# Kernel optimization log

Measured on AMD Instinct MI355X. Metric: run time of the kernel, lower is better.

Reference implementation:

```python
import jax, jax.numpy as jnp
import numpy as np

B, N, C, H = 8, 1024, 768, 12
HD = C // H  # 64
SCALE = HD ** -0.5
T = 4
N_HALF = T // 2  # loop body with attention runs N_HALF times, V accumulates T times


def setup_inputs() -> dict:
    key = jax.random.key(0)
    ks = jax.random.split(key, 8)
    s = 0.02
    return {
        "x": jax.random.normal(ks[0], (B, N, C), jnp.float32),
        "Wqkv": jax.random.normal(ks[1], (3 * C, C), jnp.float32) * s,
        "Wfc1": jax.random.normal(ks[2], (HD, HD), jnp.float32) * s,
        "bfc1": jax.random.normal(ks[3], (HD,), jnp.float32) * s,
        "Wfc2": jax.random.normal(ks[4], (HD, HD), jnp.float32) * s,
        "bfc2": jax.random.normal(ks[5], (HD,), jnp.float32) * s,
        "Wproj": jax.random.normal(ks[6], (C, C), jnp.float32) * s,
        "bproj": jax.random.normal(ks[7], (C,), jnp.float32) * s,
    }


def reference(x, Wqkv, Wfc1, bfc1, Wfc2, bfc2, Wproj, bproj):
    b, n, c = x.shape
    # qkv projection (no bias), split into per-head q,k,v: [B,H,N,hd]
    qkv = (x @ Wqkv.T).reshape(b, n, 3, H, HD).transpose(2, 0, 3, 1, 4)
    q, k, v = qkv[0], qkv[1], qkv[2]
    # Loop body is stateless per timestep: first N_HALF steps each add the same
    # att_spk; all T steps add the same relu(v). Compute once, scale by counts.
    Q_spk = jax.nn.relu(q) @ Wfc1.T + bfc1  # [B,H,N,hd]
    K_spk = jax.nn.relu(k) @ Wfc2.T + bfc2  # [B,H,N,hd]
    att_spk = jax.nn.relu(jnp.einsum("bhqd,bhkd->bhqk", Q_spk, K_spk) * SCALE)
    att_rec = att_spk * float(N_HALF)   # accumulated over t < T/2
    V_rec = jax.nn.relu(v) * float(T)   # accumulated over all T steps
    att = jax.nn.softmax(att_rec, axis=-1)
    out = jnp.einsum("bhqk,bhkd->bhqd", att, V_rec)  # [B,H,N,hd]
    out = out.transpose(0, 2, 1, 3).reshape(b, n, c)
    return out @ Wproj.T + bproj
```

## Files before the change

kernel.cpp:

```cpp
#include <hip/hip_runtime.h>
#include <hip/hip_bf16.h>
#include <stdint.h>
#include <math.h>

#define BB   8
#define NN_  1024
#define CC   768
#define HH   12
#define HDD  64

typedef __attribute__((ext_vector_type(8))) short bf16x8;
typedef __attribute__((ext_vector_type(4))) float f32x4;
typedef __attribute__((ext_vector_type(16))) float f32x16;
typedef __attribute__((ext_vector_type(4))) float f32x4v;
typedef __attribute__((ext_vector_type(4))) unsigned short u16x4;

union FragU { unsigned int u[4]; bf16x8 b; };

__device__ __forceinline__ unsigned short f2bf(float f) {
    union { float f; unsigned int u; } v; v.f = f;
    unsigned int r = v.u + 0x7fffu + ((v.u >> 16) & 1u);
    return (unsigned short)(r >> 16);
}

#define CVTPK(d_, a_, b_) asm("v_cvt_pk_bf16_f32 %0, %1, %2" : "=v"(d_) : "v"(a_), "v"(b_))
#define SWAP32(a_, b_) asm("v_permlane32_swap_b32 %0, %1" : "+v"(a_), "+v"(b_))

#define GLDS(g_, l_) __builtin_amdgcn_global_load_lds( \
    (const __attribute__((address_space(1))) void*)(g_), \
    (__attribute__((address_space(3))) void*)(l_), 16, 0, 0)

#define MKFRAGS(P_, F0_, F1_) do {                                             \
    unsigned int c0,c1,c2,c3,c4,c5,c6,c7;                                      \
    CVTPK(c0, P_[0],  P_[1]);  CVTPK(c1, P_[2],  P_[3]);                       \
    CVTPK(c2, P_[4],  P_[5]);  CVTPK(c3, P_[6],  P_[7]);                       \
    CVTPK(c4, P_[8],  P_[9]);  CVTPK(c5, P_[10], P_[11]);                      \
    CVTPK(c6, P_[12], P_[13]); CVTPK(c7, P_[14], P_[15]);                      \
    SWAP32(c0, c2); SWAP32(c1, c3); SWAP32(c4, c6); SWAP32(c5, c7);            \
    FragU fu0_, fu1_;                                                          \
    fu0_.u[0]=c0; fu0_.u[1]=c1; fu0_.u[2]=c2; fu0_.u[3]=c3;                    \
    fu1_.u[0]=c4; fu1_.u[1]=c5; fu1_.u[2]=c6; fu1_.u[3]=c7;                    \
    F0_ = fu0_.b; F1_ = fu1_.b;                                                \
} while (0)

#define CVT_N0 1572864
#define CVT_N1 2015232
#define CVT_N2 2162688
#define CVT_N3 2163712
#define CVT_N4 2164736
__global__ void cvt_all(const float* __restrict__ x, const float* __restrict__ wqkv,
                        const float* __restrict__ wproj, const float* __restrict__ wf1,
                        const float* __restrict__ wf2,
                        unsigned short* __restrict__ xb, unsigned short* __restrict__ wqkvb,
                        unsigned short* __restrict__ wprojb, unsigned short* __restrict__ wf1b,
                        unsigned short* __restrict__ wf2b) {
    int i = blockIdx.x * blockDim.x + threadIdx.x;
    int stride = gridDim.x * blockDim.x;
    for (; i < CVT_N4; i += stride) {
        const f32x4v* src; u16x4* dst; int off;
        if (i < CVT_N0)      { src = (const f32x4v*)x;     dst = (u16x4*)xb;     off = i; }
        else if (i < CVT_N1) { src = (const f32x4v*)wqkv;  dst = (u16x4*)wqkvb;  off = i - CVT_N0; }
        else if (i < CVT_N2) { src = (const f32x4v*)wproj; dst = (u16x4*)wprojb; off = i - CVT_N1; }
        else if (i < CVT_N3) { src = (const f32x4v*)wf1;   dst = (u16x4*)wf1b;   off = i - CVT_N2; }
        else                 { src = (const f32x4v*)wf2;   dst = (u16x4*)wf2b;   off = i - CVT_N3; }
        f32x4v v = src[off];
        u16x4 o;
        o.x = f2bf(v.x); o.y = f2bf(v.y); o.z = f2bf(v.z); o.w = f2bf(v.w);
        dst[off] = o;
    }
}

__global__ __launch_bounds__(256)
void qkv_spk_gemm(const unsigned short* __restrict__ X,
                  const unsigned short* __restrict__ Wqkv,
                  const unsigned short* __restrict__ Wf1,
                  const unsigned short* __restrict__ Wf2,
                  const float* __restrict__ bf1,
                  const float* __restrict__ bf2,
                  unsigned short* __restrict__ Rq,
                  unsigned short* __restrict__ Rk,
                  unsigned short* __restrict__ VT) {
    __shared__ short sX[128 * 32];
    __shared__ short sW[128 * 32];
    const int K = 768;
    const int t    = threadIdx.x;
    const int wid  = t >> 6;
    const int lane = t & 63;
    const int l31  = lane & 31;
    const int hi5  = lane >> 5;
    const int th = (wid & 1) * 64;
    const int fh = (wid >> 1) * 64;
    const int brow = blockIdx.x * 128;
    const int bcol = blockIdx.y * 128;

    const int srow = t >> 2;
    const int scol = ((t & 3) ^ (srow & 3)) * 8;

#define QSTG(k0_) do {                                                         \
    _Pragma("unroll")                                                          \
    for (int i = 0; i < 2; i++) {                                              \
        int row_ = srow + i * 64;                                              \
        GLDS(X    + (size_t)(brow + row_) * K + (k0_) + scol,                  \
             &sX[(i * 256 + wid * 64) * 8]);                                   \
        GLDS(Wqkv + (size_t)(bcol + row_) * K + (k0_) + scol,                  \
             &sW[(i * 256 + wid * 64) * 8]);                                   \
    }                                                                          \
} while (0)

    f32x16 acc[2][2];
#pragma unroll
    for (int fb = 0; fb < 2; fb++)
#pragma unroll
        for (int tb = 0; tb < 2; tb++)
#pragma unroll
            for (int r = 0; r < 16; r++) acc[fb][tb][r] = 0.f;

    for (int k0 = 0; k0 < K; k0 += 32) {
        QSTG(k0);
        __syncthreads();
        const char* cw = (const char*)sW;
        const char* cx = (const char*)sX;
        bf16x8 wf[2][2], xf[2][2];
#pragma unroll
        for (int fb = 0; fb < 2; fb++) {
            int row = fh + fb * 32 + l31;
            const char* rb = cw + row * 64;
#pragma unroll
            for (int kk = 0; kk < 2; kk++)
                wf[fb][kk] = *(const bf16x8*)(rb + (((kk * 2 + hi5) ^ (row & 3)) << 4));
        }
#pragma unroll
        for (int tb = 0; tb < 2; tb++) {
            int row = th + tb * 32 + l31;
            const char* rb = cx + row * 64;
#pragma unroll
            for (int kk = 0; kk < 2; kk++)
                xf[tb][kk] = *(const bf16x8*)(rb + (((kk * 2 + hi5) ^ (row & 3)) << 4));
        }
#pragma unroll
        for (int kk = 0; kk < 2; kk++)
#pragma unroll
            for (int fb = 0; fb < 2; fb++)
#pragma unroll
                for (int tb = 0; tb < 2; tb++)
                    acc[fb][tb] = __builtin_amdgcn_mfma_f32_32x32x16_bf16(
                        wf[fb][kk], xf[tb][kk], acc[fb][tb], 0, 0, 0);
        __syncthreads();
    }
#undef QSTG

    const int fbase = bcol + fh;
    const int p  = fbase / 768;
    const int hh = (fbase - p * 768) >> 6;
    const int tok0 = brow + th;
    const int b  = tok0 >> 10;
    const int n0 = tok0 & 1023;
    const int crow0 = 4 * hi5;

    if (p == 2) {
        const size_t vtb = ((size_t)(b * HH + hh)) * HDD * NN_;
#pragma unroll
        for (int fb = 0; fb < 2; fb++)
#pragma unroll
            for (int tb = 0; tb < 2; tb++)
#pragma unroll
                for (int r = 0; r < 16; r++) {
                    int d = fb * 32 + (r & 3) + 8 * (r >> 2) + crow0;
                    int n = n0 + tb * 32 + l31;
                    VT[vtb + (size_t)d * NN_ + n] = f2bf(4.f * fmaxf(acc[fb][tb][r], 0.f));
                }
    } else {
        const unsigned short* Wf = p ? Wf2 : Wf1;
        const float* bfp = p ? bf2 : bf1;
        unsigned short* R = p ? Rk : Rq;
        bf16x8 wfr[2][4];
#pragma unroll
        for (int dh = 0; dh < 2; dh++)
#pragma unroll
            for (int ks = 0; ks < 4; ks++)
                wfr[dh][ks] = *(const bf16x8*)&Wf[(size_t)(dh * 32 + l31) * HDD + ks * 16 + hi5 * 8];
        float bv0 = bfp[l31], bv1 = bfp[32 + l31];
        const size_t qkb = ((size_t)(b * HH + hh)) * NN_ * HDD;
#pragma unroll
        for (int tb = 0; tb < 2; tb++) {
            float pv0[16], pv1[16];
#pragma unroll
            for (int r = 0; r < 16; r++) {
                pv0[r] = fmaxf(acc[0][tb][r], 0.f);
                pv1[r] = fmaxf(acc[1][tb][r], 0.f);
            }
            bf16x8 pa0, pa1, pa2, pa3;
            MKFRAGS(pv0, pa0, pa1);
            MKFRAGS(pv1, pa2, pa3);
            f32x16 D0, D1;
#pragma unroll
            for (int r = 0; r < 16; r++) { D0[r] = 0.f; D1[r] = 0.f; }
            D0 = __builtin_amdgcn_mfma_f32_32x32x16_bf16(pa0, wfr[0][0], D0, 0, 0, 0);
            D0 = __builtin_amdgcn_mfma_f32_32x32x16_bf16(pa1, wfr[0][1], D0, 0, 0, 0);
            D0 = __builtin_amdgcn_mfma_f32_32x32x16_bf16(pa2, wfr[0][2], D0, 0, 0, 0);
            D0 = __builtin_amdgcn_mfma_f32_32x32x16_bf16(pa3, wfr[0][3], D0, 0, 0, 0);
            D1 = __builtin_amdgcn_mfma_f32_32x32x16_bf16(pa0, wfr[1][0], D1, 0, 0, 0);
            D1 = __builtin_amdgcn_mfma_f32_32x32x16_bf16(pa1, wfr[1][1], D1, 0, 0, 0);
            D1 = __builtin_amdgcn_mfma_f32_32x32x16_bf16(pa2, wfr[1][2], D1, 0, 0, 0);
            D1 = __builtin_amdgcn_mfma_f32_32x32x16_bf16(pa3, wfr[1][3], D1, 0, 0, 0);
#pragma unroll
            for (int r = 0; r < 16; r++) {
                int n = n0 + tb * 32 + (r & 3) + 8 * (r >> 2) + crow0;
                size_t rowb = qkb + (size_t)n * HDD;
                R[rowb + l31]      = f2bf(D0[r] + bv0);
                R[rowb + 32 + l31] = f2bf(D1[r] + bv1);
            }
        }
    }
}

__global__ __launch_bounds__(256, 2)
void attn_kernel(const unsigned short* __restrict__ Q,
                 const unsigned short* __restrict__ Kx,
                 const unsigned short* __restrict__ VT,
                 unsigned short* __restrict__ AO) {
    __shared__ short sK[2][64 * 64];
    __shared__ short sV[2][64 * 64];
    __shared__ float sinv[4][32];

    const int t    = threadIdx.x;
    const int lane = t & 63;
    const int wid  = t >> 6;
    const int l31  = lane & 31;
    const int hi5  = lane >> 5;

    const int bid = (int)blockIdx.x;
    const int lbid = (bid & 7) * 96 + (bid >> 3);
    const int bh = lbid >> 3;
    const int qt = lbid & 7;
    const int b = bh / HH, h = bh - b * HH;

    const unsigned short* Qs = Q  + (size_t)bh * NN_ * HDD;
    const unsigned short* Ks = Kx + (size_t)bh * NN_ * HDD;
    const unsigned short* Vt = VT + (size_t)bh * HDD * NN_;
    const int q0 = qt * 128 + wid * 32;

    bf16x8 qf[4];
#pragma unroll
    for (int ds = 0; ds < 4; ds++)
        qf[ds] = *(const bf16x8*)&Qs[(size_t)(q0 + l31) * HDD + ds * 16 + hi5 * 8];

    f32x16 O0, O1;
#pragma unroll
    for (int r = 0; r < 16; r++) { O0[r] = 0.f; O1[r] = 0.f; }
    float sumacc = 0.f;

    const int srow = t >> 3;
    const int sslot = t & 7;
    const int dstoff = ((t & 192)) * 8;

#define STAGE(buf_, kt_) do {                                                  \
    _Pragma("unroll")                                                          \
    for (int i = 0; i < 2; i++) {                                              \
        int row_ = srow + i * 32;                                              \
        int sl_  = (sslot ^ (row_ & 7)) << 3;                                  \
        const unsigned short* gk_ = Ks + (size_t)((kt_) * 64 + row_) * HDD + sl_; \
        const unsigned short* gv_ = Vt + (size_t)row_ * NN_ + (kt_) * 64 + sl_;   \
        GLDS(gk_, &sK[buf_][i * 2048 + dstoff]);                               \
        GLDS(gv_, &sV[buf_][i * 2048 + dstoff]);                               \
    }                                                                          \
} while (0)

    STAGE(0, 0);
    __syncthreads();

    int buf = 0;
    for (int kt = 0; kt < 16; ++kt) {
        if (kt < 15) STAGE(buf ^ 1, kt + 1);

        const char* kbase = (const char*)&sK[buf][0];
        const char* vbase = (const char*)&sV[buf][0];

        bf16x8 vbf[4][2];
#pragma unroll
        for (int ks = 0; ks < 4; ks++)
#pragma unroll
            for (int dt = 0; dt < 2; dt++) {
                int d = dt * 32 + l31;
                vbf[ks][dt] = *(const bf16x8*)(vbase + d * 128 +
                               ((ks * 32 + hi5 * 16) ^ ((d & 7) << 4)));
            }
        bf16x8 ka[2][4];
#pragma unroll
        for (int kt2 = 0; kt2 < 2; kt2++)
#pragma unroll
            for (int ds = 0; ds < 4; ds++) {
                int kk = kt2 * 32 + l31;
                ka[kt2][ds] = *(const bf16x8*)(kbase + kk * 128 +
                               ((ds * 32 + hi5 * 16) ^ ((kk & 7) << 4)));
            }

        f32x16 S0, S1;
#pragma unroll
        for (int r = 0; r < 16; r++) { S0[r] = 0.f; S1[r] = 0.f; }
#pragma unroll
        for (int ds = 0; ds < 4; ds++) {
            S0 = __builtin_amdgcn_mfma_f32_32x32x16_bf16(ka[0][ds], qf[ds], S0, 0, 0, 0);
            S1 = __builtin_amdgcn_mfma_f32_32x32x16_bf16(ka[1][ds], qf[ds], S1, 0, 0, 0);
        }

        float p0[16], p1[16];
#pragma unroll
        for (int r = 0; r < 16; r++) {
            p0[r] = exp2f(0.36067376f * fmaxf(S0[r], 0.f));
            p1[r] = exp2f(0.36067376f * fmaxf(S1[r], 0.f));
        }
        float s0 = 0.f, s1 = 0.f;
#pragma unroll
        for (int r = 0; r < 16; r++) { s0 += p0[r]; s1 += p1[r]; }
        sumacc += s0 + s1;

        bf16x8 paf0, paf1, paf2, paf3;
        MKFRAGS(p0, paf0, paf1);
        MKFRAGS(p1, paf2, paf3);

        O0 = __builtin_amdgcn_mfma_f32_32x32x16_bf16(paf0, vbf[0][0], O0, 0, 0, 0);
        O1 = __builtin_amdgcn_mfma_f32_32x32x16_bf16(paf0, vbf[0][1], O1, 0, 0, 0);
        O0 = __builtin_amdgcn_mfma_f32_32x32x16_bf16(paf1, vbf[1][0], O0, 0, 0, 0);
        O1 = __builtin_amdgcn_mfma_f32_32x32x16_bf16(paf1, vbf[1][1], O1, 0, 0, 0);
        O0 = __builtin_amdgcn_mfma_f32_32x32x16_bf16(paf2, vbf[2][0], O0, 0, 0, 0);
        O1 = __builtin_amdgcn_mfma_f32_32x32x16_bf16(paf2, vbf[2][1], O1, 0, 0, 0);
        O0 = __builtin_amdgcn_mfma_f32_32x32x16_bf16(paf3, vbf[3][0], O0, 0, 0, 0);
        O1 = __builtin_amdgcn_mfma_f32_32x32x16_bf16(paf3, vbf[3][1], O1, 0, 0, 0);

        __syncthreads();
        buf ^= 1;
    }
#undef STAGE

    float stot = sumacc + __shfl_xor(sumacc, 32, 64);
    float inv = 1.f / stot;
    if (l31 == lane) sinv[wid][l31] = inv;
    __syncthreads();

#pragma unroll
    for (int r = 0; r < 16; r++) {
        int qloc = (r & 3) + 8 * (r >> 2) + 4 * hi5;
        float iv = sinv[wid][qloc];
        size_t row = (size_t)(b * NN_ + q0 + qloc) * CC + h * HDD;
        AO[row + l31]      = f2bf(O0[r] * iv);
        AO[row + 32 + l31] = f2bf(O1[r] * iv);
    }
}

__global__ __launch_bounds__(256)
void proj_gemm(const unsigned short* __restrict__ A,
               const unsigned short* __restrict__ Bt,
               const float* __restrict__ bias,
               float* __restrict__ Out) {
    __shared__ short sA[128 * 32];
    __shared__ short sB[128 * 32];
    const int K = 768;
    const int lane = threadIdx.x & 63;
    const int wid  = threadIdx.x >> 6;
    const int wr = wid >> 1, wc = wid & 1;
    const int brow = blockIdx.x * 128;
    const int bcol = blockIdx.y * 128;
    const int t = threadIdx.x;

    f32x4 acc[4][4];
#pragma unroll
    for (int m = 0; m < 4; m++)
#pragma unroll
        for (int n = 0; n < 4; n++) acc[m][n] = (f32x4){0.f, 0.f, 0.f, 0.f};

    for (int k0 = 0; k0 < K; k0 += 32) {
#pragma unroll
        for (int i = 0; i < 2; i++) {
            int tt  = i * 256 + t;
            int row = tt >> 2;
            int kc  = (tt & 3) * 8;
            const unsigned short* ga = A  + (size_t)(brow + row) * K + k0 + kc;
            const unsigned short* gb = Bt + (size_t)(bcol + row) * K + k0 + kc;
            GLDS(ga, &sA[(i * 256 + wid * 64) * 8]);
            GLDS(gb, &sB[(i * 256 + wid * 64) * 8]);
        }
        __syncthreads();
        bf16x8 af[4], bfg[4];
#pragma unroll
        for (int m = 0; m < 4; m++) {
            int r = wr * 64 + m * 16 + (lane & 15);
            af[m] = *(const bf16x8*)&sA[r * 32 + (lane >> 4) * 8];
        }
#pragma unroll
        for (int n = 0; n < 4; n++) {
            int c = wc * 64 + n * 16 + (lane & 15);
            bfg[n] = *(const bf16x8*)&sB[c * 32 + (lane >> 4) * 8];
        }
#pragma unroll
        for (int m = 0; m < 4; m++)
#pragma unroll
            for (int n = 0; n < 4; n++)
                acc[m][n] = __builtin_amdgcn_mfma_f32_16x16x32_bf16(af[m], bfg[n], acc[m][n], 0, 0, 0);
        __syncthreads();
    }
#pragma unroll
    for (int m = 0; m < 4; m++)
#pragma unroll
        for (int n = 0; n < 4; n++) {
            int col = bcol + wc * 64 + n * 16 + (lane & 15);
            float bv = bias[col];
#pragma unroll
            for (int r = 0; r < 4; r++) {
                int row = brow + wr * 64 + m * 16 + (lane >> 4) * 4 + r;
                Out[(size_t)row * 768 + col] = acc[m][n][r] + bv;
            }
        }
}

extern "C" void kernel_launch(void* const* d_in, const int* in_sizes, int n_in,
                              void* d_out, int out_size, void* d_ws, size_t ws_size,
                              hipStream_t stream) {
    const float* x     = (const float*)d_in[0];
    const float* Wqkv  = (const float*)d_in[1];
    const float* Wfc1  = (const float*)d_in[2];
    const float* bfc1  = (const float*)d_in[3];
    const float* Wfc2  = (const float*)d_in[4];
    const float* bfc2  = (const float*)d_in[5];
    const float* Wproj = (const float*)d_in[6];
    const float* bproj = (const float*)d_in[7];
    float* out = (float*)d_out;

    char* ws = (char*)d_ws;
    const size_t SZ_XN = (size_t)8192 * 768 * 2;
    unsigned short* x_bf    = (unsigned short*)ws; ws += SZ_XN;
    unsigned short* wqkv_bf = (unsigned short*)ws; ws += (size_t)2304 * 768 * 2;
    unsigned short* wproj_bf= (unsigned short*)ws; ws += (size_t)768 * 768 * 2;
    unsigned short* wfc1_bf = (unsigned short*)ws; ws += 64 * 64 * 2;
    unsigned short* wfc2_bf = (unsigned short*)ws; ws += 64 * 64 * 2;
    unsigned short* Rq      = (unsigned short*)ws; ws += SZ_XN;
    unsigned short* Rk      = (unsigned short*)ws; ws += SZ_XN;
    unsigned short* VT      = (unsigned short*)ws; ws += SZ_XN;

    cvt_all<<<2048, 256, 0, stream>>>(x, Wqkv, Wproj, Wfc1, Wfc2,
                                      x_bf, wqkv_bf, wproj_bf, wfc1_bf, wfc2_bf);
    qkv_spk_gemm<<<dim3(64, 18), 256, 0, stream>>>(x_bf, wqkv_bf, wfc1_bf, wfc2_bf,
                                                   bfc1, bfc2, Rq, Rk, VT);
    attn_kernel<<<768, 256, 0, stream>>>(Rq, Rk, VT, x_bf);
    proj_gemm<<<dim3(64, 6), 256, 0, stream>>>(x_bf, wproj_bf, bproj, out);
}
```

Before: 144.9 us.

## Restructure QKV GEMM with 256x128 tiles, triple-buffered LDS pipeline, and XCD-aware block mapping

Rewrites the QKV projection GEMM to use 512-thread blocks with 256x128 output tiles and BK=64. Global-to-LDS loads run through a three-stage ring buffer, issued two tiles ahead and waited on with vmcnt, so there is one barrier per tile instead of two. The block index is remapped across the 8 XCDs for better L2 locality, and MFMA priority is raised with setprio. This trades higher LDS use (about 144KB) and one block per CU for fewer syncs and more overlap of loads with compute.

```diff
diff --git a/kernel.cpp b/kernel.cpp
--- a/kernel.cpp
+++ b/kernel.cpp
@@ -70,7 +70,7 @@
     }
 }
 
-__global__ __launch_bounds__(256)
+__global__ __launch_bounds__(512, 1)
 void qkv_spk_gemm(const unsigned short* __restrict__ X,
                   const unsigned short* __restrict__ Wqkv,
                   const unsigned short* __restrict__ Wf1,
@@ -80,30 +80,39 @@
                   unsigned short* __restrict__ Rq,
                   unsigned short* __restrict__ Rk,
                   unsigned short* __restrict__ VT) {
-    __shared__ short sX[128 * 32];
-    __shared__ short sW[128 * 32];
-    const int K = 768;
+    __shared__ short sA[3][256 * 64];
+    __shared__ short sB[3][128 * 64];
+
     const int t    = threadIdx.x;
     const int wid  = t >> 6;
     const int lane = t & 63;
     const int l31  = lane & 31;
     const int hi5  = lane >> 5;
-    const int th = (wid & 1) * 64;
-    const int fh = (wid >> 1) * 64;
-    const int brow = blockIdx.x * 128;
-    const int bcol = blockIdx.y * 128;
-
-    const int srow = t >> 2;
-    const int scol = ((t & 3) ^ (srow & 3)) * 8;
-
-#define QSTG(k0_) do {                                                         \
+    const int fw   = wid >> 1;
+    const int wn   = wid & 1;
+
+    const int bid  = (int)blockIdx.x;
+    const int lbid = (bid & 7) * 72 + (bid >> 3);
+    const int bx   = lbid & 63;
+    const int by   = lbid >> 6;
+    const int F0   = by * 256;
+    const int T0   = bx * 128;
+
+#define STG(bi_, kt_) do {                                                     \
+    const int k0_ = (kt_) * 64;                                                \
+    _Pragma("unroll")                                                          \
+    for (int i = 0; i < 4; i++) {                                              \
+        int li_ = i * 512 + t;                                                 \
+        int row_ = li_ >> 3, sl_ = li_ & 7;                                    \
+        GLDS(Wqkv + (size_t)(F0 + row_) * 768 + k0_ + ((sl_ ^ (row_ & 7)) * 8),\
+             &sA[bi_][li_ * 8]);                                               \
+    }                                                                          \
     _Pragma("unroll")                                                          \
     for (int i = 0; i < 2; i++) {                                              \
-        int row_ = srow + i * 64;                                              \
-        GLDS(X    + (size_t)(brow + row_) * K + (k0_) + scol,                  \
-             &sX[(i * 256 + wid * 64) * 8]);                                   \
-        GLDS(Wqkv + (size_t)(bcol + row_) * K + (k0_) + scol,                  \
-             &sW[(i * 256 + wid * 64) * 8]);                                   \
+        int li_ = i * 512 + t;                                                 \
+        int row_ = li_ >> 3, sl_ = li_ & 7;                                    \
+        GLDS(X + (size_t)(T0 + row_) * 768 + k0_ + ((sl_ ^ (row_ & 7)) * 8),   \
+             &sB[bi_][li_ * 8]);                                               \
     }                                                                          \
 } while (0)
 
@@ -115,44 +124,59 @@
 #pragma unroll
             for (int r = 0; r < 16; r++) acc[fb][tb][r] = 0.f;
 
-    for (int k0 = 0; k0 < K; k0 += 32) {
-        QSTG(k0);
-        __syncthreads();
-        const char* cw = (const char*)sW;
-        const char* cx = (const char*)sX;
-        bf16x8 wf[2][2], xf[2][2];
-#pragma unroll
-        for (int fb = 0; fb < 2; fb++) {
-            int row = fh + fb * 32 + l31;
-            const char* rb = cw + row * 64;
-#pragma unroll
-            for (int kk = 0; kk < 2; kk++)
-                wf[fb][kk] = *(const bf16x8*)(rb + (((kk * 2 + hi5) ^ (row & 3)) << 4));
-        }
-#pragma unroll
-        for (int tb = 0; tb < 2; tb++) {
-            int row = th + tb * 32 + l31;
-            const char* rb = cx + row * 64;
-#pragma unroll
-            for (int kk = 0; kk < 2; kk++)
-                xf[tb][kk] = *(const bf16x8*)(rb + (((kk * 2 + hi5) ^ (row & 3)) << 4));
-        }
-#pragma unroll
-        for (int kk = 0; kk < 2; kk++)
-#pragma unroll
-            for (int fb = 0; fb < 2; fb++)
-#pragma unroll
-                for (int tb = 0; tb < 2; tb++)
-                    acc[fb][tb] = __builtin_amdgcn_mfma_f32_32x32x16_bf16(
-                        wf[fb][kk], xf[tb][kk], acc[fb][tb], 0, 0, 0);
-        __syncthreads();
-    }
-#undef QSTG
-
-    const int fbase = bcol + fh;
+#define TILE(bc_, kt_) do {                                                    \
+    if ((kt_) + 2 < 12) STG(((bc_) + 2) % 3, (kt_) + 2);                       \
+    const char* ab_ = (const char*)sA[bc_];                                    \
+    const char* bb_ = (const char*)sB[bc_];                                    \
+    bf16x8 wf_[2][4], xf_[2][4];                                               \
+    _Pragma("unroll")                                                          \
+    for (int fb = 0; fb < 2; fb++) {                                           \
+        int r_ = fw * 64 + fb * 32 + l31;                                      \
+        _Pragma("unroll")                                                      \
+        for (int ks = 0; ks < 4; ks++)                                         \
+            wf_[fb][ks] = *(const bf16x8*)(ab_ + r_ * 128 +                    \
+                (((ks * 2 + hi5) ^ (r_ & 7)) << 4));                           \
+    }                                                                          \
+    _Pragma("unroll")                                                          \
+    for (int tb = 0; tb < 2; tb++) {                                           \
+        int r_ = wn * 64 + tb * 32 + l31;                                      \
+        _Pragma("unroll")                                                      \
+        for (int ks = 0; ks < 4; ks++)                                         \
+            xf_[tb][ks] = *(const bf16x8*)(bb_ + r_ * 128 +                    \
+                (((ks * 2 + hi5) ^ (r_ & 7)) << 4));                           \
+    }                                                                          \
+    __builtin_amdgcn_s_setprio(1);                                             \
+    _Pragma("unroll")                                                          \
+    for (int ks = 0; ks < 4; ks++)                                             \
+        _Pragma("unroll")                                                      \
+        for (int fb = 0; fb < 2; fb++)                                         \
+            _Pragma("unroll")                                                  \
+            for (int tb = 0; tb < 2; tb++)                                     \
+                acc[fb][tb] = __builtin_amdgcn_mfma_f32_32x32x16_bf16(         \
+                    wf_[fb][ks], xf_[tb][ks], acc[fb][tb], 0, 0, 0);           \
+    __builtin_amdgcn_s_setprio(0);                                             \
+    asm volatile("s_waitcnt vmcnt(6)" ::: "memory");                           \
+    __builtin_amdgcn_s_barrier();                                              \
+} while (0)
+
+    STG(0, 0);
+    STG(1, 1);
+    asm volatile("s_waitcnt vmcnt(6)" ::: "memory");
+    __builtin_amdgcn_s_barrier();
+
+#pragma unroll 1
+    for (int kt3 = 0; kt3 < 12; kt3 += 3) {
+        TILE(0, kt3);
+        TILE(1, kt3 + 1);
+        TILE(2, kt3 + 2);
+    }
+#undef TILE
+#undef STG
+
+    const int fbase = F0 + fw * 64;
     const int p  = fbase / 768;
     const int hh = (fbase - p * 768) >> 6;
-    const int tok0 = brow + th;
+    const int tok0 = T0 + wn * 64;
     const int b  = tok0 >> 10;
     const int n0 = tok0 & 1023;
     const int crow0 = 4 * hi5;
@@ -439,8 +463,8 @@
 
     cvt_all<<<2048, 256, 0, stream>>>(x, Wqkv, Wproj, Wfc1, Wfc2,
                                       x_bf, wqkv_bf, wproj_bf, wfc1_bf, wfc2_bf);
-    qkv_spk_gemm<<<dim3(64, 18), 256, 0, stream>>>(x_bf, wqkv_bf, wfc1_bf, wfc2_bf,
-                                                   bfc1, bfc2, Rq, Rk, VT);
+    qkv_spk_gemm<<<576, 512, 0, stream>>>(x_bf, wqkv_bf, wfc1_bf, wfc2_bf,
+                                          bfc1, bfc2, Rq, Rk, VT);
     attn_kernel<<<768, 256, 0, stream>>>(Rq, Rk, VT, x_bf);
     proj_gemm<<<dim3(64, 6), 256, 0, stream>>>(x_bf, wproj_bf, bproj, out);
 }
```

After: 138.7 us. -4.2%, faster.
